# Performance work log

Hardware: AMD Instinct MI355X
Metric: run time of the kernel (lower is better)

## Reference

```python
import jax, jax.numpy as jnp
import numpy as np

B, F, D = 1024, 256, 64  # batch, featureNumb, featureDim


def setup_inputs() -> dict:
    key = jax.random.key(0)
    k1, k2, k3, k4 = jax.random.split(key, 4)
    feature = jax.random.normal(k1, (B, F, D), dtype=jnp.float32)
    indicator = jax.random.normal(k2, (F, D), dtype=jnp.float32)
    # QKVTransformV2(n, D, D): n stacked DxD linear maps of the indicator
    W_qk = jax.random.normal(k3, (2, D, D), dtype=jnp.float32) / np.float32(np.sqrt(D))
    W_qkv = jax.random.normal(k4, (3, D, D), dtype=jnp.float32) / np.float32(np.sqrt(D))
    return {"feature": feature, "indicator": indicator, "W_qk": W_qk, "W_qkv": W_qkv}


def reference(feature, indicator, W_qk, W_qkv):
    d = indicator.shape[-1]
    scale = jnp.asarray(1.0 / np.sqrt(d), feature.dtype)

    # --- gate branch: QKTrans + DotWeight + LTE (straight-through hard threshold) ---
    trans = jnp.einsum('fd,nde->nfe', indicator, W_qk)            # [2,F,D]
    gate_logits = jnp.einsum('id,jd->ij', trans[0], trans[1]) * scale  # [F,F]
    gate = (gate_logits > 0).astype(feature.dtype)                # LTE forward: hard 0/1 gate

    # --- QKV branch, fused form of the rank-1 outer products ---
    # Original: QKV_outer[t,i,j] = qkv[t,i] (x) qkv[t,j]  (DxD rank-1)
    #           input[b,t,i,j,:] = feature[b,i] @ QKV_outer[t,i,j]
    #                            = (feature[b,i] . qkv[t,i]) * qkv[t,j]
    qkv = jnp.einsum('fd,nde->nfe', indicator, W_qkv)             # [3,F,D]
    s = jnp.einsum('bfd,nfd->nbf', feature, qkv)                  # s[t,b,i] = feature[b,i].qkv[t,i]

    # score[b,i,j] = input[b,0,i,j,:] . input[b,1,j,i,:]
    #              = s[0,b,i] * s[1,b,j] * (qkv[1,i] . qkv[0,j])
    cross = jnp.einsum('id,jd->ij', qkv[1], qkv[0])               # [F,F]
    score = s[0][:, :, None] * s[1][:, None, :] * cross[None]     # [B,F,F]
    scoreHat = score * gate[None]                                 # [B,F,F]

    # output[b,i,:] = sum_j scoreHat[b,i,j] * value[b,i,j,:]
    #               = s[2,b,i] * sum_j scoreHat[b,i,j] * qkv[2,j,:]
    out = s[2][:, :, None] * jnp.einsum('bij,jd->bid', scoreHat, qkv[2])  # [B,F,D]
    return out
```

## Files before the change

kernel.cpp:

```cpp
#include <hip/hip_runtime.h>
#include <stdint.h>

#define B 1024
#define F 256
#define D 64

typedef __attribute__((ext_vector_type(8))) short short8;
typedef __attribute__((ext_vector_type(4))) float f32x4;

__device__ __forceinline__ short f2bf(float f) {
    unsigned u = __builtin_bit_cast(unsigned, f);
    u += 0x7fff + ((u >> 16) & 1);
    return (short)(u >> 16);
}
__device__ __forceinline__ float bf2f(short s) {
    unsigned u = ((unsigned)(unsigned short)s) << 16;
    return __builtin_bit_cast(float, u);
}
__device__ __forceinline__ unsigned pk_bf16(float a, float b) {
    unsigned ua = __builtin_bit_cast(unsigned, a) + 0x8000u;
    unsigned ub = __builtin_bit_cast(unsigned, b) + 0x8000u;
    return __builtin_amdgcn_perm(ub, ua, 0x07060302u);
}


__global__ void precompute_trans(const float* __restrict__ indicator,
                                 const float* __restrict__ W_qk,
                                 const float* __restrict__ W_qkv,
                                 float* __restrict__ trans,
                                 float* __restrict__ qkv) {
    int idx = blockIdx.x * blockDim.x + threadIdx.x;
    int n   = idx / (F * D);
    int rem = idx - n * (F * D);
    int f   = rem / D;
    int e   = rem - f * D;
    const float* W = (n < 2) ? (W_qk + n * D * D) : (W_qkv + (n - 2) * D * D);
    const float* ind = indicator + f * D;
    float acc = 0.f;
#pragma unroll 8
    for (int d = 0; d < D; ++d) acc += ind[d] * W[d * D + e];
    if (n < 2) trans[n * F * D + f * D + e] = acc;
    else       qkv[(n - 2) * F * D + f * D + e] = acc;
}

__global__ __launch_bounds__(256) void compute_Mt(const float* __restrict__ trans,
                                                  const float* __restrict__ qkv,
                                                  short* __restrict__ At,
                                                  short* __restrict__ q2K) {
    int j = blockIdx.x;
    int i = threadIdx.x;
    const float4* t0 = (const float4*)(trans + i * D);
    const float4* t1 = (const float4*)(trans + F * D + j * D);
    const float4* q1 = (const float4*)(qkv + F * D + i * D);
    const float4* q0 = (const float4*)(qkv + j * D);
    float d0 = 0.f, d1 = 0.f;
#pragma unroll
    for (int k = 0; k < D / 4; ++k) {
        float4 a = t0[k], b = t1[k], c = q1[k], e = q0[k];
        d0 += a.x * b.x + a.y * b.y + a.z * b.z + a.w * b.w;
        d1 += c.x * e.x + c.y * e.y + c.z * e.z + c.w * e.w;
    }
    float v = (d0 > 0.f) ? d1 : 0.f;
    At[((j >> 5) * F + i) * 32 + (j & 31)] = f2bf(v);
    if (j < D) q2K[((i >> 5) * D + j) * 32 + (i & 31)] = f2bf(qkv[2 * F * D + i * D + j]);
}

__global__ __launch_bounds__(256, 2) void fused_main(const float* __restrict__ feature,
                                                     const float* __restrict__ qkv,
                                                     const short* __restrict__ At,
                                                     const short* __restrict__ q2K,
                                                     float* __restrict__ out) {
    int bp = blockIdx.x;
    int b0 = bp * 2;
    int tid = threadIdx.x;

    __shared__ __align__(16) short s1L[2 * F];
    __shared__ float gL[2 * F];

    {
        int rg = tid >> 4;
        int l  = tid & 15;
#pragma unroll 4
        for (int p = 0; p < 16; ++p) {
            int f = p * 16 + rg;
            float4 fv0 = ((const float4*)(feature + ((size_t)(b0 * F + f)) * D))[l];
            float4 fv1 = ((const float4*)(feature + ((size_t)((b0 + 1) * F + f)) * D))[l];
            float4 q0 = ((const float4*)(qkv + f * D))[l];
            float4 q1 = ((const float4*)(qkv + F * D + f * D))[l];
            float4 q2 = ((const float4*)(qkv + 2 * F * D + f * D))[l];
            float a00 = fv0.x * q0.x + fv0.y * q0.y + fv0.z * q0.z + fv0.w * q0.w;
            float a01 = fv0.x * q1.x + fv0.y * q1.y + fv0.z * q1.z + fv0.w * q1.w;
            float a02 = fv0.x * q2.x + fv0.y * q2.y + fv0.z * q2.z + fv0.w * q2.w;
            float a10 = fv1.x * q0.x + fv1.y * q0.y + fv1.z * q0.z + fv1.w * q0.w;
            float a11 = fv1.x * q1.x + fv1.y * q1.y + fv1.z * q1.z + fv1.w * q1.w;
            float a12 = fv1.x * q2.x + fv1.y * q2.y + fv1.z * q2.z + fv1.w * q2.w;
#pragma unroll
            for (int m = 1; m < 16; m <<= 1) {
                a00 += __shfl_xor(a00, m, 64);
                a01 += __shfl_xor(a01, m, 64);
                a02 += __shfl_xor(a02, m, 64);
                a10 += __shfl_xor(a10, m, 64);
                a11 += __shfl_xor(a11, m, 64);
                a12 += __shfl_xor(a12, m, 64);
            }
            if (l == 0) {
                gL[f]       = a00 * a02;
                gL[F + f]   = a10 * a12;
                s1L[f]      = f2bf(a01);
                s1L[F + f]  = f2bf(a11);
            }
        }
    }
    __syncthreads();

    int wave = tid >> 6;
    int lane = tid & 63;
    int wr   = wave >> 1, wc = wave & 1;
    int l16  = lane & 15;
    int lq   = lane >> 4;
    int kq   = lq * 8;
    int b    = b0 + wc;

    f32x4 acc[8][4];
#pragma unroll
    for (int mt = 0; mt < 8; ++mt)
#pragma unroll
        for (int nt = 0; nt < 4; ++nt) acc[mt][nt] = (f32x4){0.f, 0.f, 0.f, 0.f};

    for (int jt = 0; jt < F / 32; ++jt) {
        short8 sv = *(const short8*)(s1L + wc * F + jt * 32 + kq);
        float sf[8];
#pragma unroll
        for (int e = 0; e < 8; ++e) sf[e] = bf2f(sv[e]);

        short8 bfr[4];
#pragma unroll
        for (int nt = 0; nt < 4; ++nt) {
            int d = nt * 16 + l16;
            short8 qv = *(const short8*)(q2K + (jt * D + d) * 32 + kq);
            int4 packed;
            packed.x = pk_bf16(bf2f(qv[0]) * sf[0], bf2f(qv[1]) * sf[1]);
            packed.y = pk_bf16(bf2f(qv[2]) * sf[2], bf2f(qv[3]) * sf[3]);
            packed.z = pk_bf16(bf2f(qv[4]) * sf[4], bf2f(qv[5]) * sf[5]);
            packed.w = pk_bf16(bf2f(qv[6]) * sf[6], bf2f(qv[7]) * sf[7]);
            bfr[nt] = __builtin_bit_cast(short8, packed);
        }
#pragma unroll
        for (int mt = 0; mt < 8; ++mt) {
            int i = wr * 128 + mt * 16 + l16;
            short8 af = *(const short8*)(At + ((size_t)jt * F + i) * 32 + kq);
#pragma unroll
            for (int nt = 0; nt < 4; ++nt)
                acc[mt][nt] = __builtin_amdgcn_mfma_f32_16x16x32_bf16(
                    af, bfr[nt], acc[mt][nt], 0, 0, 0);
        }
    }

#pragma unroll
    for (int mt = 0; mt < 8; ++mt) {
#pragma unroll
        for (int r = 0; r < 4; ++r) {
            int i = wr * 128 + mt * 16 + lq * 4 + r;
            float gg = gL[wc * F + i];
            float* orow = out + ((size_t)(b * F + i)) * D;
#pragma unroll
            for (int nt = 0; nt < 4; ++nt)
                orow[nt * 16 + l16] = gg * acc[mt][nt][r];
        }
    }
}

extern "C" void kernel_launch(void* const* d_in, const int* in_sizes, int n_in,
                              void* d_out, int out_size, void* d_ws, size_t ws_size,
                              hipStream_t stream) {
    const float* feature   = (const float*)d_in[0];
    const float* indicator = (const float*)d_in[1];
    const float* W_qk      = (const float*)d_in[2];
    const float* W_qkv     = (const float*)d_in[3];
    float* out = (float*)d_out;

    float* ws    = (float*)d_ws;
    float* trans = ws;
    float* qkv   = trans + 2 * F * D;
    short* At    = (short*)(qkv + 3 * F * D);
    short* q2K   = At + F * F;

    hipLaunchKernelGGL(precompute_trans, dim3((5 * F * D) / 256), dim3(256), 0,
                       stream, indicator, W_qk, W_qkv, trans, qkv);
    hipLaunchKernelGGL(compute_Mt, dim3(F), dim3(F), 0, stream, trans, qkv, At, q2K);
    hipLaunchKernelGGL(fused_main, dim3(B / 2), dim3(256), 0, stream,
                       feature, qkv, At, q2K, out);
}
```

Baseline: 143.2 us.

## Split s-projection into separate kernel and tile GEMM with LDS-staged At/q2K

```diff
diff --git a/kernel.cpp b/kernel.cpp
--- a/kernel.cpp
+++ b/kernel.cpp
@@ -65,70 +65,89 @@
     if (j < D) q2K[((i >> 5) * D + j) * 32 + (i & 31)] = f2bf(qkv[2 * F * D + i * D + j]);
 }
 
-__global__ __launch_bounds__(256, 2) void fused_main(const float* __restrict__ feature,
-                                                     const float* __restrict__ qkv,
-                                                     const short* __restrict__ At,
-                                                     const short* __restrict__ q2K,
-                                                     float* __restrict__ out) {
-    int bp = blockIdx.x;
-    int b0 = bp * 2;
+__global__ __launch_bounds__(256) void compute_s(const float* __restrict__ feature,
+                                                 const float* __restrict__ qkv,
+                                                 float* __restrict__ gS,
+                                                 short* __restrict__ s1S) {
+    int b0 = blockIdx.x * 2;
+    int rg = threadIdx.x >> 4;
+    int l  = threadIdx.x & 15;
+#pragma unroll 4
+    for (int p = 0; p < 16; ++p) {
+        int f = p * 16 + rg;
+        float4 fv0 = ((const float4*)(feature + ((size_t)(b0 * F + f)) * D))[l];
+        float4 fv1 = ((const float4*)(feature + ((size_t)((b0 + 1) * F + f)) * D))[l];
+        float4 q0 = ((const float4*)(qkv + f * D))[l];
+        float4 q1 = ((const float4*)(qkv + F * D + f * D))[l];
+        float4 q2 = ((const float4*)(qkv + 2 * F * D + f * D))[l];
+        float a00 = fv0.x * q0.x + fv0.y * q0.y + fv0.z * q0.z + fv0.w * q0.w;
+        float a01 = fv0.x * q1.x + fv0.y * q1.y + fv0.z * q1.z + fv0.w * q1.w;
+        float a02 = fv0.x * q2.x + fv0.y * q2.y + fv0.z * q2.z + fv0.w * q2.w;
+        float a10 = fv1.x * q0.x + fv1.y * q0.y + fv1.z * q0.z + fv1.w * q0.w;
+        float a11 = fv1.x * q1.x + fv1.y * q1.y + fv1.z * q1.z + fv1.w * q1.w;
+        float a12 = fv1.x * q2.x + fv1.y * q2.y + fv1.z * q2.z + fv1.w * q2.w;
+#pragma unroll
+        for (int m = 1; m < 16; m <<= 1) {
+            a00 += __shfl_xor(a00, m, 64);
+            a01 += __shfl_xor(a01, m, 64);
+            a02 += __shfl_xor(a02, m, 64);
+            a10 += __shfl_xor(a10, m, 64);
+            a11 += __shfl_xor(a11, m, 64);
+            a12 += __shfl_xor(a12, m, 64);
+        }
+        if (l == 0) {
+            gS[b0 * F + f]        = a00 * a02;
+            gS[(b0 + 1) * F + f]  = a10 * a12;
+            s1S[b0 * F + f]       = f2bf(a01);
+            s1S[(b0 + 1) * F + f] = f2bf(a11);
+        }
+    }
+}
+
+__global__ __launch_bounds__(512, 4) void gemm_out(const short* __restrict__ At,
+                                                   const short* __restrict__ q2K,
+                                                   const float* __restrict__ gS,
+                                                   const short* __restrict__ s1S,
+                                                   float* __restrict__ out) {
+    int it  = blockIdx.x & 3;
+    int bg  = blockIdx.x >> 2;
     int tid = threadIdx.x;
 
-    __shared__ __align__(16) short s1L[2 * F];
-    __shared__ float gL[2 * F];
+    __shared__ __align__(16) short AtL[8 * 64 * 32];
+    __shared__ __align__(16) short q2L[8 * 64 * 32];
 
     {
-        int rg = tid >> 4;
-        int l  = tid & 15;
-#pragma unroll 4
-        for (int p = 0; p < 16; ++p) {
-            int f = p * 16 + rg;
-            float4 fv0 = ((const float4*)(feature + ((size_t)(b0 * F + f)) * D))[l];
-            float4 fv1 = ((const float4*)(feature + ((size_t)((b0 + 1) * F + f)) * D))[l];
-            float4 q0 = ((const float4*)(qkv + f * D))[l];
-            float4 q1 = ((const float4*)(qkv + F * D + f * D))[l];
-            float4 q2 = ((const float4*)(qkv + 2 * F * D + f * D))[l];
-            float a00 = fv0.x * q0.x + fv0.y * q0.y + fv0.z * q0.z + fv0.w * q0.w;
-            float a01 = fv0.x * q1.x + fv0.y * q1.y + fv0.z * q1.z + fv0.w * q1.w;
-            float a02 = fv0.x * q2.x + fv0.y * q2.y + fv0.z * q2.z + fv0.w * q2.w;
-            float a10 = fv1.x * q0.x + fv1.y * q0.y + fv1.z * q0.z + fv1.w * q0.w;
-            float a11 = fv1.x * q1.x + fv1.y * q1.y + fv1.z * q1.z + fv1.w * q1.w;
-            float a12 = fv1.x * q2.x + fv1.y * q2.y + fv1.z * q2.z + fv1.w * q2.w;
-#pragma unroll
-            for (int m = 1; m < 16; m <<= 1) {
-                a00 += __shfl_xor(a00, m, 64);
-                a01 += __shfl_xor(a01, m, 64);
-                a02 += __shfl_xor(a02, m, 64);
-                a10 += __shfl_xor(a10, m, 64);
-                a11 += __shfl_xor(a11, m, 64);
-                a12 += __shfl_xor(a12, m, 64);
-            }
-            if (l == 0) {
-                gL[f]       = a00 * a02;
-                gL[F + f]   = a10 * a12;
-                s1L[f]      = f2bf(a01);
-                s1L[F + f]  = f2bf(a11);
-            }
-        }
+        const float4* Ag = (const float4*)At;
+        const float4* Qg = (const float4*)q2K;
+        float4* Al = (float4*)AtL;
+        float4* Ql = (float4*)q2L;
+#pragma unroll
+        for (int v = tid; v < 2048; v += 512) {
+            int jt = v >> 8, k = v & 255;
+            Al[v] = Ag[jt * 1024 + it * 256 + k];
+        }
+#pragma unroll
+        for (int v = tid; v < 2048; v += 512) Ql[v] = Qg[v];
     }
     __syncthreads();
 
-    int wave = tid >> 6;
+    int w    = tid >> 6;
     int lane = tid & 63;
-    int wr   = wave >> 1, wc = wave & 1;
     int l16  = lane & 15;
     int lq   = lane >> 4;
     int kq   = lq * 8;
-    int b    = b0 + wc;
-
-    f32x4 acc[8][4];
-#pragma unroll
-    for (int mt = 0; mt < 8; ++mt)
+    int b    = bg * 8 + w;
+
+    const short* s1b = s1S + b * F;
+
+    f32x4 acc[4][4];
+#pragma unroll
+    for (int mt = 0; mt < 4; ++mt)
 #pragma unroll
         for (int nt = 0; nt < 4; ++nt) acc[mt][nt] = (f32x4){0.f, 0.f, 0.f, 0.f};
 
     for (int jt = 0; jt < F / 32; ++jt) {
-        short8 sv = *(const short8*)(s1L + wc * F + jt * 32 + kq);
+        short8 sv = *(const short8*)(s1b + jt * 32 + kq);
         float sf[8];
 #pragma unroll
         for (int e = 0; e < 8; ++e) sf[e] = bf2f(sv[e]);
@@ -137,7 +156,7 @@
 #pragma unroll
         for (int nt = 0; nt < 4; ++nt) {
             int d = nt * 16 + l16;
-            short8 qv = *(const short8*)(q2K + (jt * D + d) * 32 + kq);
+            short8 qv = *(const short8*)(q2L + (jt * 64 + d) * 32 + kq);
             int4 packed;
             packed.x = pk_bf16(bf2f(qv[0]) * sf[0], bf2f(qv[1]) * sf[1]);
             packed.y = pk_bf16(bf2f(qv[2]) * sf[2], bf2f(qv[3]) * sf[3]);
@@ -146,9 +165,8 @@
             bfr[nt] = __builtin_bit_cast(short8, packed);
         }
 #pragma unroll
-        for (int mt = 0; mt < 8; ++mt) {
-            int i = wr * 128 + mt * 16 + l16;
-            short8 af = *(const short8*)(At + ((size_t)jt * F + i) * 32 + kq);
+        for (int mt = 0; mt < 4; ++mt) {
+            short8 af = *(const short8*)(AtL + (jt * 64 + mt * 16 + l16) * 32 + kq);
 #pragma unroll
             for (int nt = 0; nt < 4; ++nt)
                 acc[mt][nt] = __builtin_amdgcn_mfma_f32_16x16x32_bf16(
@@ -156,16 +174,18 @@
         }
     }
 
-#pragma unroll
-    for (int mt = 0; mt < 8; ++mt) {
-#pragma unroll
-        for (int r = 0; r < 4; ++r) {
-            int i = wr * 128 + mt * 16 + lq * 4 + r;
-            float gg = gL[wc * F + i];
-            float* orow = out + ((size_t)(b * F + i)) * D;
-#pragma unroll
-            for (int nt = 0; nt < 4; ++nt)
-                orow[nt * 16 + l16] = gg * acc[mt][nt][r];
+    const float4* g4 = (const float4*)(gS + b * F + it * 64);
+#pragma unroll
+    for (int mt = 0; mt < 4; ++mt) {
+        float4 gg = g4[mt * 4 + lq];
+        float* obase = out + ((size_t)(b * F + it * 64 + mt * 16 + lq * 4)) * D;
+#pragma unroll
+        for (int nt = 0; nt < 4; ++nt) {
+            float* o = obase + nt * 16 + l16;
+            o[0 * D] = gg.x * acc[mt][nt][0];
+            o[1 * D] = gg.y * acc[mt][nt][1];
+            o[2 * D] = gg.z * acc[mt][nt][2];
+            o[3 * D] = gg.w * acc[mt][nt][3];
         }
     }
 }
@@ -182,12 +202,16 @@
     float* ws    = (float*)d_ws;
     float* trans = ws;
     float* qkv   = trans + 2 * F * D;
-    short* At    = (short*)(qkv + 3 * F * D);
+    float* gS    = qkv + 3 * F * D;
+    short* At    = (short*)(gS + B * F);
     short* q2K   = At + F * F;
+    short* s1S   = q2K + (F / 32) * D * 32;
 
     hipLaunchKernelGGL(precompute_trans, dim3((5 * F * D) / 256), dim3(256), 0,
                        stream, indicator, W_qk, W_qkv, trans, qkv);
     hipLaunchKernelGGL(compute_Mt, dim3(F), dim3(F), 0, stream, trans, qkv, At, q2K);
-    hipLaunchKernelGGL(fused_main, dim3(B / 2), dim3(256), 0, stream,
-                       feature, qkv, At, q2K, out);
-}
+    hipLaunchKernelGGL(compute_s, dim3(B / 2), dim3(256), 0, stream,
+                       feature, qkv, gS, s1S);
+    hipLaunchKernelGGL(gemm_out, dim3((B / 8) * 4), dim3(512), 0, stream,
+                       At, q2K, gS, s1S, out);
+}
```

Measured after the change: 146.2 us. 2.1% more time.
